# Kernel tuning notes

Measured on AMD Instinct MI355X. Metric: run time of the kernel, lower is better.

The kernel has to match this reference:

```python
import jax, jax.numpy as jnp
import numpy as np

D_MODEL = 1024
N_HEADS = 16
D_KEYS = 64
GROUP_POSITIONS = [list(range(g * 32, (g + 1) * 32)) for g in range(4)]


def _make_tables(group_positions, dim):
    # InGroup table: pe[j,i] = (j/Lg) * L0 / 10000^(2*(i//2)/dim)
    L0 = len(group_positions[0])
    rows = []
    for grp in group_positions:
        Lg = len(grp)
        for j in range(Lg):
            rows.append([j / Lg * L0 / np.power(10000.0, 2 * (i // 2) / dim) for i in range(dim)])
    pe = np.array(rows)
    ingroup = np.concatenate([np.sin(pe[:, 0::2]), np.cos(pe[:, 1::2])], axis=1).astype(np.float32)
    # Sequence (group) table: pe[j,i] = grp[0] / 10000^(j/Lg), constant over i
    rows = []
    for grp in group_positions:
        Lg = len(grp)
        for j in range(Lg):
            rows.append([grp[0] / np.power(10000.0, j / Lg) for _ in range(dim)])
    pe = np.array(rows)
    seq = np.concatenate([np.sin(pe[:, 0::2]), np.cos(pe[:, 1::2])], axis=1).astype(np.float32)
    return jnp.asarray(ingroup), jnp.asarray(seq)


def setup_inputs() -> dict:
    key = jax.random.key(0)
    ks = jax.random.split(key, 12)
    B, L, S = 64, 128, 128
    dqk = D_KEYS * N_HEADS
    sc_in = 1.0 / np.sqrt(D_MODEL)
    sc_out = 1.0 / np.sqrt(dqk)
    inp = {
        "queries": jax.random.normal(ks[0], (B, L, D_MODEL), jnp.float32),
        "keys": jax.random.normal(ks[1], (B, S, D_MODEL), jnp.float32),
        "values": jax.random.normal(ks[2], (B, S, D_MODEL), jnp.float32),
        "attn_mask": jnp.zeros((B, 1, L, S), dtype=bool),
        "Wq": jax.random.normal(ks[3], (D_MODEL, dqk), jnp.float32) * sc_in,
        "bq": jnp.zeros((dqk,), jnp.float32),
        "Wk": jax.random.normal(ks[4], (D_MODEL, dqk), jnp.float32) * sc_in,
        "bk": jnp.zeros((dqk,), jnp.float32),
        "Wv": jax.random.normal(ks[5], (D_MODEL, dqk), jnp.float32) * sc_in,
        "bv": jnp.zeros((dqk,), jnp.float32),
        "Wo": jax.random.normal(ks[6], (dqk, D_MODEL), jnp.float32) * sc_out,
        "bo": jnp.zeros((D_MODEL,), jnp.float32),
    }
    pos_ingroup, pos_seq = _make_tables(GROUP_POSITIONS, D_KEYS)
    inp["pos_ingroup"] = pos_ingroup  # [n_pos, d_keys]
    inp["pos_seq"] = pos_seq          # [n_pos, d_keys]
    return inp


def _rope(x, pos):
    # x: [B, H, L, D]; pos: [L, D]
    sin, cos = jnp.split(pos, 2, axis=-1)
    sin_pos = jnp.stack([sin, sin], axis=-1).reshape(pos.shape)
    cos_pos = jnp.stack([cos, cos], axis=-1).reshape(pos.shape)
    rot = jnp.stack([-x[..., 1::2], x[..., ::2]], axis=-1).reshape(x.shape)
    return x * cos_pos + rot * sin_pos


def reference(queries, keys, values, attn_mask, Wq, bq, Wk, bk, Wv, bv, Wo, bo, pos_ingroup, pos_seq):
    B, L, _ = queries.shape
    S = keys.shape[1]
    H, E = N_HEADS, D_KEYS
    q = (queries @ Wq + bq).reshape(B, L, H, E).transpose(0, 2, 1, 3)  # [B,H,L,E]
    k = (keys @ Wk + bk).reshape(B, S, H, E).transpose(0, 2, 1, 3)
    v = (values @ Wv + bv).reshape(B, S, H, E).transpose(0, 2, 1, 3)
    # group-sequence in-group RoPE, then group RoPE (tables gathered at arange positions)
    q = _rope(_rope(q, pos_ingroup[:L]), pos_seq[:L])
    k = _rope(_rope(k, pos_ingroup[:S]), pos_seq[:S])
    # inner full attention on [B,L,H,E] layout
    scale = 1.0 / jnp.sqrt(jnp.asarray(E, q.dtype))
    scores = jnp.einsum("bhle,bhse->bhls", q, k) * scale
    scores = jnp.where(attn_mask, jnp.asarray(-jnp.inf, scores.dtype), scores)
    attn = jax.nn.softmax(scores, axis=-1)  # [B,H,L,S]
    out = jnp.einsum("bhls,bhsd->blhd", attn, v).reshape(B, L, H * E)
    return out @ Wo + bo, attn
```

## Files before the change

kernel.cpp:

```cpp
#include <hip/hip_runtime.h>
#include <cstdint>

typedef float f32x4 __attribute__((ext_vector_type(4)));
typedef __bf16 bf16x8 __attribute__((ext_vector_type(8)));
typedef unsigned short u16x8 __attribute__((ext_vector_type(8)));

typedef __attribute__((address_space(3))) uint32_t lds_u32;
typedef __attribute__((address_space(1))) const uint32_t glb_u32;

#define GLOAD_LDS16(gp, lp) \
  __builtin_amdgcn_global_load_lds((glb_u32*)(uintptr_t)(gp), (lds_u32*)(uintptr_t)(lp), 16, 0, 0)

__device__ inline unsigned short f2bf(float f) {
  union { float f; uint32_t u; } v; v.f = f;
  uint32_t u = v.u;
  return (unsigned short)((u + 0x7fffu + ((u >> 16) & 1u)) >> 16);
}

__global__ void prep_w(const float* __restrict__ wq, const float* __restrict__ wk,
                       const float* __restrict__ wv, const float* __restrict__ wo,
                       unsigned short* __restrict__ wt)
{
  __shared__ float t[64][65];
  const int z = blockIdx.z;
  const float* W = (z == 0) ? wq : (z == 1) ? wk : (z == 2) ? wv : wo;
  unsigned short* Wt = wt + (size_t)z * 1048576;
  const int n0 = blockIdx.x * 64, k0 = blockIdx.y * 64;
  const int tx = threadIdx.x & 63, ty = threadIdx.x >> 6;
#pragma unroll
  for (int i = 0; i < 16; i++) {
    int row = i * 4 + ty;
    t[row][tx] = W[(size_t)(k0 + row) * 1024 + n0 + tx];
  }
  __syncthreads();
#pragma unroll
  for (int i = 0; i < 16; i++) {
    int row = i * 4 + ty;
    Wt[(size_t)(n0 + row) * 1024 + k0 + tx] = f2bf(t[tx][row]);
  }
}

__global__ void comb_kernel(const float* __restrict__ ing, const float* __restrict__ seq,
                            float* __restrict__ cosc, float* __restrict__ sinc)
{
  int idx = blockIdx.x * 256 + threadIdx.x;
  int j = idx >> 5, i = idx & 31;
  float s1 = ing[j * 64 + i], c1 = ing[j * 64 + 32 + i];
  float s2 = seq[j * 64 + i], c2 = seq[j * 64 + 32 + i];
  cosc[idx] = c1 * c2 - s1 * s2;
  sinc[idx] = s1 * c2 + c1 * s2;
}

__global__ void cvt_kernel(const float* __restrict__ q, const float* __restrict__ k,
                           const float* __restrict__ v, unsigned short* __restrict__ dst)
{
  const int z = blockIdx.z;
  const float* src = (z == 0) ? q : (z == 1) ? k : v;
  unsigned short* d = dst + (size_t)z * 8388608;
  size_t i = ((size_t)blockIdx.x * 256 + threadIdx.x) * 4;
  float4 f = *(const float4*)&src[i];
  ushort4 o;
  o.x = f2bf(f.x); o.y = f2bf(f.y); o.z = f2bf(f.z); o.w = f2bf(f.w);
  *(ushort4*)&d[i] = o;
}

__global__ __launch_bounds__(256, 2)
void gemm_bt(const unsigned short* __restrict__ Abase,
             const unsigned short* __restrict__ Bbase,
             const float* __restrict__ b0, const float* __restrict__ b1,
             const float* __restrict__ b2,
             unsigned short* __restrict__ qb, unsigned short* __restrict__ kb,
             unsigned short* __restrict__ vtb,
             float* __restrict__ outf,
             const float* __restrict__ cosc, const float* __restrict__ sinc,
             int final_mode)
{
  __shared__ __attribute__((aligned(16))) unsigned short Sh[2][8192];
  unsigned short* As = &Sh[0][0];
  unsigned short* Bs = &Sh[1][0];

  const int tid = threadIdx.x;
  const int lane = tid & 63;
  const int wave = tid >> 6;
  const int quad = lane >> 4;
  const int l15 = lane & 15;

  const int z = blockIdx.z;
  const int tileM = blockIdx.x * 128;
  const int tileN = blockIdx.y * 128;
  const int K = 1024;

  const unsigned short* A = Abase + (size_t)z * (8192u * 1024u);
  const unsigned short* B = Bbase + (size_t)z * (1024u * 1024u);

  const int wm = (wave >> 1) * 64;
  const int wn = (wave & 1) * 64;

  f32x4 acc[4][4];
#pragma unroll
  for (int a = 0; a < 4; a++)
#pragma unroll
    for (int n = 0; n < 4; n++)
      acc[a][n] = (f32x4){0.f, 0.f, 0.f, 0.f};

  for (int k0 = 0; k0 < K; k0 += 64) {
#pragma unroll
    for (int cc = 0; cc < 4; cc++) {
      int c = wave * 4 + cc;
      int s = c * 64 + lane;
      int row = s >> 3;
      int gc = (s & 7) ^ (row & 7);
      const unsigned short* ga = A + (size_t)(tileM + row) * K + k0 + gc * 8;
      const unsigned short* gb = B + (size_t)(tileN + row) * K + k0 + gc * 8;
      GLOAD_LDS16(ga, &As[c * 512]);
      GLOAD_LDS16(gb, &Bs[c * 512]);
    }
    __syncthreads();

#pragma unroll
    for (int ks = 0; ks < 2; ks++) {
      bf16x8 af[4], bfr[4];
#pragma unroll
      for (int a = 0; a < 4; a++) {
        int r = wm + a * 16 + l15;
        int cp = (ks * 4 + quad) ^ (r & 7);
        af[a] = *(const bf16x8*)&As[(r * 8 + cp) * 8];
      }
#pragma unroll
      for (int n = 0; n < 4; n++) {
        int r = wn + n * 16 + l15;
        int cp = (ks * 4 + quad) ^ (r & 7);
        bfr[n] = *(const bf16x8*)&Bs[(r * 8 + cp) * 8];
      }
#pragma unroll
      for (int a = 0; a < 4; a++)
#pragma unroll
        for (int n = 0; n < 4; n++)
          acc[a][n] = __builtin_amdgcn_mfma_f32_16x16x32_bf16(af[a], bfr[n], acc[a][n], 0, 0, 0);
    }
    __syncthreads();
  }

  if (final_mode) {
#pragma unroll
    for (int n = 0; n < 4; n++) {
      int cg = tileN + wn + n * 16 + l15;
      float bias = b0[cg];
#pragma unroll
      for (int a = 0; a < 4; a++)
#pragma unroll
        for (int reg = 0; reg < 4; reg++) {
          int r = tileM + wm + a * 16 + quad * 4 + reg;
          outf[(size_t)r * 1024 + cg] = acc[a][n][reg] + bias;
        }
    }
  } else {
    const float* bias = (z == 0) ? b0 : (z == 1) ? b1 : b2;
    unsigned short* outq = (z == 0) ? qb : kb;
    unsigned short* flat = &Sh[0][0];

#pragma unroll
    for (int n = 0; n < 4; n++) {
      int lcg = wn + n * 16 + l15;
      float bv_ = bias[tileN + lcg];
      int e = lcg & 63;
#pragma unroll
      for (int a = 0; a < 4; a++)
#pragma unroll
        for (int reg = 0; reg < 4; reg++) {
          int l = wm + a * 16 + quad * 4 + reg;
          float v = acc[a][n][reg] + bv_;
          unsigned short ov;
          int f;
          if (z == 2) {
            ov = f2bf(v);
            f = lcg * 128 + l;
            f ^= ((f >> 7) & 15) << 3;
          } else {
            float other = __shfl_xor(v, 1);
            float cs = cosc[l * 32 + (e >> 1)];
            float sn = sinc[l * 32 + (e >> 1)];
            ov = f2bf(v * cs + ((e & 1) ? other : -other) * sn);
            f = ((lcg >> 6) << 13) + (l << 6) + e;
            f ^= ((f >> 8) & 7) << 3;
          }
          flat[f] = ov;
        }
    }
    __syncthreads();

    unsigned short* gout = ((z == 2) ? vtb : outq) +
                           ((size_t)(tileM >> 7) * 16 + (tileN >> 6)) * 8192;
#pragma unroll
    for (int c = 0; c < 8; c++) {
      int f0 = tid * 64 + c * 8;
      int s0 = (z == 2) ? (f0 ^ (((f0 >> 7) & 15) << 3))
                        : (f0 ^ (((f0 >> 8) & 7) << 3));
      *(u16x8*)&gout[f0] = *(const u16x8*)&flat[s0];
    }
  }
}

__global__ __launch_bounds__(256, 2)
void attn_kernel(const unsigned short* __restrict__ qb,
                 const unsigned short* __restrict__ kb,
                 const unsigned short* __restrict__ vtb,
                 const unsigned char* __restrict__ mask,
                 float* __restrict__ attn_out,
                 unsigned short* __restrict__ ob)
{
  __shared__ __attribute__((aligned(16))) unsigned short Pb[128 * 136];
  const int tid = threadIdx.x;
  const int lane = tid & 63;
  const int wave = tid >> 6;
  const int quad = lane >> 4;
  const int l15 = lane & 15;
  const int bh = blockIdx.x;
  const int b = bh >> 4;
  const int h = bh & 15;

  const unsigned short* q = qb + (size_t)bh * 128 * 64;
  const unsigned short* k = kb + (size_t)bh * 128 * 64;
  const unsigned short* vt = vtb + (size_t)bh * 64 * 128;

  f32x4 sacc[2][8];
#pragma unroll
  for (int mt = 0; mt < 2; mt++)
#pragma unroll
    for (int nt = 0; nt < 8; nt++)
      sacc[mt][nt] = (f32x4){0.f, 0.f, 0.f, 0.f};

#pragma unroll
  for (int ks = 0; ks < 2; ks++) {
    bf16x8 aq[2], bk[8];
#pragma unroll
    for (int mt = 0; mt < 2; mt++)
      aq[mt] = *(const bf16x8*)&q[(size_t)(wave * 32 + mt * 16 + l15) * 64 + ks * 32 + quad * 8];
#pragma unroll
    for (int nt = 0; nt < 8; nt++)
      bk[nt] = *(const bf16x8*)&k[(size_t)(nt * 16 + l15) * 64 + ks * 32 + quad * 8];
#pragma unroll
    for (int mt = 0; mt < 2; mt++)
#pragma unroll
      for (int nt = 0; nt < 8; nt++)
        sacc[mt][nt] = __builtin_amdgcn_mfma_f32_16x16x32_bf16(aq[mt], bk[nt], sacc[mt][nt], 0, 0, 0);
  }

  const float scale = 0.125f;
#pragma unroll
  for (int mt = 0; mt < 2; mt++) {
#pragma unroll
    for (int reg = 0; reg < 4; reg++) {
      int r = wave * 32 + mt * 16 + quad * 4 + reg;
      const unsigned char* mrow = mask + ((size_t)b * 128 + r) * 128;
      float sv[8];
#pragma unroll
      for (int nt = 0; nt < 8; nt++) {
        float x = sacc[mt][nt][reg] * scale;
        if (mrow[nt * 16 + l15]) x = -__builtin_inff();
        sv[nt] = x;
      }
      float m = sv[0];
#pragma unroll
      for (int nt = 1; nt < 8; nt++) m = fmaxf(m, sv[nt]);
#pragma unroll
      for (int off = 1; off < 16; off <<= 1) m = fmaxf(m, __shfl_xor(m, off));
      float s = 0.f;
#pragma unroll
      for (int nt = 0; nt < 8; nt++) { sv[nt] = __expf(sv[nt] - m); s += sv[nt]; }
#pragma unroll
      for (int off = 1; off < 16; off <<= 1) s += __shfl_xor(s, off);
      float inv = 1.0f / s;
      float* arow = attn_out + ((size_t)bh * 128 + r) * 128;
#pragma unroll
      for (int nt = 0; nt < 8; nt++) {
        float p = sv[nt] * inv;
        arow[nt * 16 + l15] = p;
        Pb[r * 136 + nt * 16 + l15] = f2bf(p);
      }
    }
  }
  __syncthreads();

  f32x4 oacc[2][4];
#pragma unroll
  for (int mt = 0; mt < 2; mt++)
#pragma unroll
    for (int nt = 0; nt < 4; nt++)
      oacc[mt][nt] = (f32x4){0.f, 0.f, 0.f, 0.f};

#pragma unroll
  for (int ks = 0; ks < 4; ks++) {
    bf16x8 bv[4], ap[2];
#pragma unroll
    for (int nt = 0; nt < 4; nt++)
      bv[nt] = *(const bf16x8*)&vt[(size_t)(nt * 16 + l15) * 128 + ks * 32 + quad * 8];
#pragma unroll
    for (int mt = 0; mt < 2; mt++)
      ap[mt] = *(const bf16x8*)&Pb[(size_t)(wave * 32 + mt * 16 + l15) * 136 + ks * 32 + quad * 8];
#pragma unroll
    for (int mt = 0; mt < 2; mt++)
#pragma unroll
      for (int nt = 0; nt < 4; nt++)
        oacc[mt][nt] = __builtin_amdgcn_mfma_f32_16x16x32_bf16(ap[mt], bv[nt], oacc[mt][nt], 0, 0, 0);
  }

#pragma unroll
  for (int mt = 0; mt < 2; mt++)
#pragma unroll
    for (int nt = 0; nt < 4; nt++)
#pragma unroll
      for (int reg = 0; reg < 4; reg++) {
        int r = wave * 32 + mt * 16 + quad * 4 + reg;
        int e = nt * 16 + l15;
        ob[((size_t)b * 128 + r) * 1024 + h * 64 + e] = f2bf(oacc[mt][nt][reg]);
      }
}

extern "C" void kernel_launch(void* const* d_in, const int* in_sizes, int n_in,
                              void* d_out, int out_size, void* d_ws, size_t ws_size,
                              hipStream_t stream)
{
  const float* queries = (const float*)d_in[0];
  const float* keys    = (const float*)d_in[1];
  const float* values  = (const float*)d_in[2];
  const unsigned char* mask = (const unsigned char*)d_in[3];
  const float* Wq = (const float*)d_in[4];
  const float* bq = (const float*)d_in[5];
  const float* Wk = (const float*)d_in[6];
  const float* bk = (const float*)d_in[7];
  const float* Wv = (const float*)d_in[8];
  const float* bv = (const float*)d_in[9];
  const float* Wo = (const float*)d_in[10];
  const float* bo = (const float*)d_in[11];
  const float* ping = (const float*)d_in[12];
  const float* pseq = (const float*)d_in[13];

  float* out  = (float*)d_out;
  float* attn = out + 8388608;
  unsigned short* Xbf = (unsigned short*)attn;

  char* ws = (char*)d_ws;
  unsigned short* Wt  = (unsigned short*)(ws);
  float* cosc = (float*)(ws + 8388608);
  float* sinc = (float*)(ws + 8388608 + 16384);
  unsigned short* qbuf = (unsigned short*)(ws + 8421376);
  unsigned short* kbuf = (unsigned short*)(ws + 8421376 + 16777216);
  unsigned short* vtbuf= (unsigned short*)(ws + 8421376 + 2*16777216);
  unsigned short* obuf = (unsigned short*)(ws + 8421376 + 3*16777216);

  prep_w<<<dim3(16, 16, 4), 256, 0, stream>>>(Wq, Wk, Wv, Wo, Wt);
  comb_kernel<<<16, 256, 0, stream>>>(ping, pseq, cosc, sinc);
  cvt_kernel<<<dim3(8192, 1, 3), 256, 0, stream>>>(queries, keys, values, Xbf);
  gemm_bt<<<dim3(64, 8, 3), 256, 0, stream>>>(Xbf, Wt, bq, bk, bv,
                                              qbuf, kbuf, vtbuf, nullptr,
                                              cosc, sinc, 0);
  attn_kernel<<<dim3(1024), 256, 0, stream>>>(qbuf, kbuf, vtbuf, mask, attn, obuf);
  gemm_bt<<<dim3(64, 8, 1), 256, 0, stream>>>(obuf, Wt + 3 * 1048576, bo, bo, bo,
                                              qbuf, kbuf, vtbuf, out,
                                              cosc, sinc, 1);
}
```

Measured before the change: 338.3 us.

## Fuse fp32-to-bf16 input conversion into QKV projection GEMM

Removes the separate conversion kernel that wrote bf16 copies of queries/keys/values, and adds a dedicated QKV GEMM that loads fp32 activations straight into LDS (swizzled) and converts to bf16 when building MFMA fragments. This drops a full read+write pass over the activations and one launch. In exchange the A tile in LDS doubles in size (fp32). Each of the 8 column-tile blocks now re-reads fp32 A, twice the bytes of the bf16 copy, and conversion work is repeated per block.

After: 345.8 us. 1.02x slower.

```diff
diff --git a/kernel.cpp b/kernel.cpp
--- a/kernel.cpp
+++ b/kernel.cpp
@@ -51,17 +51,134 @@
   sinc[idx] = s1 * c2 + c1 * s2;
 }
 
-__global__ void cvt_kernel(const float* __restrict__ q, const float* __restrict__ k,
-                           const float* __restrict__ v, unsigned short* __restrict__ dst)
-{
+__global__ __launch_bounds__(256, 2)
+void gemm_qkv(const float* __restrict__ qf, const float* __restrict__ kf,
+              const float* __restrict__ vf,
+              const unsigned short* __restrict__ Bbase,
+              const float* __restrict__ b0, const float* __restrict__ b1,
+              const float* __restrict__ b2,
+              unsigned short* __restrict__ qb, unsigned short* __restrict__ kb,
+              unsigned short* __restrict__ vtb,
+              const float* __restrict__ cosc, const float* __restrict__ sinc)
+{
+  __shared__ __attribute__((aligned(16))) float Asf[8192];
+  __shared__ __attribute__((aligned(16))) unsigned short Bs[8192];
+
+  const int tid = threadIdx.x;
+  const int lane = tid & 63;
+  const int wave = tid >> 6;
+  const int quad = lane >> 4;
+  const int l15 = lane & 15;
+
   const int z = blockIdx.z;
-  const float* src = (z == 0) ? q : (z == 1) ? k : v;
-  unsigned short* d = dst + (size_t)z * 8388608;
-  size_t i = ((size_t)blockIdx.x * 256 + threadIdx.x) * 4;
-  float4 f = *(const float4*)&src[i];
-  ushort4 o;
-  o.x = f2bf(f.x); o.y = f2bf(f.y); o.z = f2bf(f.z); o.w = f2bf(f.w);
-  *(ushort4*)&d[i] = o;
+  const int tileM = blockIdx.x * 128;
+  const int tileN = blockIdx.y * 128;
+  const int K = 1024;
+
+  const float* A = (z == 0) ? qf : (z == 1) ? kf : vf;
+  const unsigned short* B = Bbase + (size_t)z * (1024u * 1024u);
+
+  const int wm = (wave >> 1) * 64;
+  const int wn = (wave & 1) * 64;
+
+  f32x4 acc[4][4];
+#pragma unroll
+  for (int a = 0; a < 4; a++)
+#pragma unroll
+    for (int n = 0; n < 4; n++)
+      acc[a][n] = (f32x4){0.f, 0.f, 0.f, 0.f};
+
+  for (int k0 = 0; k0 < K; k0 += 64) {
+#pragma unroll
+    for (int cc = 0; cc < 8; cc++) {
+      int c = wave * 8 + cc;
+      int g = c * 64 + lane;
+      int row = g >> 4;
+      int gc = (g & 15) ^ (row & 15);
+      const float* ga = A + (size_t)(tileM + row) * 1024 + k0 + gc * 4;
+      GLOAD_LDS16(ga, &Asf[c * 256]);
+    }
+#pragma unroll
+    for (int cc = 0; cc < 4; cc++) {
+      int c = wave * 4 + cc;
+      int s = c * 64 + lane;
+      int row = s >> 3;
+      int gc = (s & 7) ^ (row & 7);
+      const unsigned short* gb = B + (size_t)(tileN + row) * K + k0 + gc * 8;
+      GLOAD_LDS16(gb, &Bs[c * 512]);
+    }
+    __syncthreads();
+
+#pragma unroll
+    for (int ks = 0; ks < 2; ks++) {
+      bf16x8 af[4], bfr[4];
+#pragma unroll
+      for (int a = 0; a < 4; a++) {
+        int r = wm + a * 16 + l15;
+        int L0 = ks * 8 + quad * 2;
+        f32x4 fa = *(const f32x4*)&Asf[(r * 16 + (L0 ^ l15)) * 4];
+        f32x4 fb = *(const f32x4*)&Asf[(r * 16 + ((L0 + 1) ^ l15)) * 4];
+        af[a] = (bf16x8){(__bf16)fa[0], (__bf16)fa[1], (__bf16)fa[2], (__bf16)fa[3],
+                         (__bf16)fb[0], (__bf16)fb[1], (__bf16)fb[2], (__bf16)fb[3]};
+      }
+#pragma unroll
+      for (int n = 0; n < 4; n++) {
+        int r = wn + n * 16 + l15;
+        int cp = (ks * 4 + quad) ^ (r & 7);
+        bfr[n] = *(const bf16x8*)&Bs[(r * 8 + cp) * 8];
+      }
+#pragma unroll
+      for (int a = 0; a < 4; a++)
+#pragma unroll
+        for (int n = 0; n < 4; n++)
+          acc[a][n] = __builtin_amdgcn_mfma_f32_16x16x32_bf16(af[a], bfr[n], acc[a][n], 0, 0, 0);
+    }
+    __syncthreads();
+  }
+
+  const float* bias = (z == 0) ? b0 : (z == 1) ? b1 : b2;
+  unsigned short* outq = (z == 0) ? qb : kb;
+  unsigned short* flat = (unsigned short*)Asf;
+
+#pragma unroll
+  for (int n = 0; n < 4; n++) {
+    int lcg = wn + n * 16 + l15;
+    float bv_ = bias[tileN + lcg];
+    int e = lcg & 63;
+#pragma unroll
+    for (int a = 0; a < 4; a++)
+#pragma unroll
+      for (int reg = 0; reg < 4; reg++) {
+        int l = wm + a * 16 + quad * 4 + reg;
+        float v = acc[a][n][reg] + bv_;
+        unsigned short ov;
+        int f;
+        if (z == 2) {
+          ov = f2bf(v);
+          f = lcg * 128 + l;
+          f ^= ((f >> 7) & 15) << 3;
+        } else {
+          float other = __shfl_xor(v, 1);
+          float cs = cosc[l * 32 + (e >> 1)];
+          float sn = sinc[l * 32 + (e >> 1)];
+          ov = f2bf(v * cs + ((e & 1) ? other : -other) * sn);
+          f = ((lcg >> 6) << 13) + (l << 6) + e;
+          f ^= ((f >> 8) & 7) << 4;
+        }
+        flat[f] = ov;
+      }
+  }
+  __syncthreads();
+
+  unsigned short* gout = ((z == 2) ? vtb : outq) +
+                         ((size_t)(tileM >> 7) * 16 + (tileN >> 6)) * 8192;
+#pragma unroll
+  for (int c = 0; c < 8; c++) {
+    int f0 = tid * 64 + c * 8;
+    int s0 = (z == 2) ? (f0 ^ (((f0 >> 7) & 15) << 3))
+                      : (f0 ^ (((f0 >> 8) & 7) << 4));
+    *(u16x8*)&gout[f0] = *(const u16x8*)&flat[s0];
+  }
 }
 
 __global__ __launch_bounds__(256, 2)
@@ -338,7 +455,6 @@
 
   float* out  = (float*)d_out;
   float* attn = out + 8388608;
-  unsigned short* Xbf = (unsigned short*)attn;
 
   char* ws = (char*)d_ws;
   unsigned short* Wt  = (unsigned short*)(ws);
@@ -351,10 +467,9 @@
 
   prep_w<<<dim3(16, 16, 4), 256, 0, stream>>>(Wq, Wk, Wv, Wo, Wt);
   comb_kernel<<<16, 256, 0, stream>>>(ping, pseq, cosc, sinc);
-  cvt_kernel<<<dim3(8192, 1, 3), 256, 0, stream>>>(queries, keys, values, Xbf);
-  gemm_bt<<<dim3(64, 8, 3), 256, 0, stream>>>(Xbf, Wt, bq, bk, bv,
-                                              qbuf, kbuf, vtbuf, nullptr,
-                                              cosc, sinc, 0);
+  gemm_qkv<<<dim3(64, 8, 3), 256, 0, stream>>>(queries, keys, values, Wt,
+                                               bq, bk, bv,
+                                               qbuf, kbuf, vtbuf, cosc, sinc);
   attn_kernel<<<dim3(1024), 256, 0, stream>>>(qbuf, kbuf, vtbuf, mask, attn, obuf);
   gemm_bt<<<dim3(64, 8, 1), 256, 0, stream>>>(obuf, Wt + 3 * 1048576, bo, bo, bo,
                                               qbuf, kbuf, vtbuf, out,
```

## Merge prep kernels into one launch, stage output GEMM stores via LDS

Applied to the files above, without the earlier changes.

The three preprocessing kernels (input bf16 conversion, weight transpose/convert, RoPE table combine) are merged into a single launch that dispatches on block index, removing two kernel launches and their gaps. The final GEMM epilogue now writes its fp32 tile into LDS in two halves and stores coalesced 16-byte vectors to global memory instead of scattered 4-byte stores. The XOR swizzle for q/k staging is also widened to shift LDS bank conflicts. The cost is extra barriers in the epilogue and branchy block dispatch in the merged kernel.

Measured after the change: 338.8 us. No clear change (+0.1%).

```diff
diff --git a/kernel.cpp b/kernel.cpp
--- a/kernel.cpp
+++ b/kernel.cpp
@@ -17,51 +17,55 @@
   return (unsigned short)((u + 0x7fffu + ((u >> 16) & 1u)) >> 16);
 }
 
-__global__ void prep_w(const float* __restrict__ wq, const float* __restrict__ wk,
-                       const float* __restrict__ wv, const float* __restrict__ wo,
-                       unsigned short* __restrict__ wt)
+__global__ void prep_all(const float* __restrict__ q, const float* __restrict__ k,
+                         const float* __restrict__ v,
+                         const float* __restrict__ wq, const float* __restrict__ wk,
+                         const float* __restrict__ wv, const float* __restrict__ wo,
+                         const float* __restrict__ ing, const float* __restrict__ seq,
+                         unsigned short* __restrict__ dst, unsigned short* __restrict__ wt,
+                         float* __restrict__ cosc, float* __restrict__ sinc)
 {
   __shared__ float t[64][65];
-  const int z = blockIdx.z;
-  const float* W = (z == 0) ? wq : (z == 1) ? wk : (z == 2) ? wv : wo;
-  unsigned short* Wt = wt + (size_t)z * 1048576;
-  const int n0 = blockIdx.x * 64, k0 = blockIdx.y * 64;
-  const int tx = threadIdx.x & 63, ty = threadIdx.x >> 6;
-#pragma unroll
-  for (int i = 0; i < 16; i++) {
-    int row = i * 4 + ty;
-    t[row][tx] = W[(size_t)(k0 + row) * 1024 + n0 + tx];
-  }
-  __syncthreads();
-#pragma unroll
-  for (int i = 0; i < 16; i++) {
-    int row = i * 4 + ty;
-    Wt[(size_t)(n0 + row) * 1024 + k0 + tx] = f2bf(t[tx][row]);
-  }
-}
-
-__global__ void comb_kernel(const float* __restrict__ ing, const float* __restrict__ seq,
-                            float* __restrict__ cosc, float* __restrict__ sinc)
-{
-  int idx = blockIdx.x * 256 + threadIdx.x;
-  int j = idx >> 5, i = idx & 31;
-  float s1 = ing[j * 64 + i], c1 = ing[j * 64 + 32 + i];
-  float s2 = seq[j * 64 + i], c2 = seq[j * 64 + 32 + i];
-  cosc[idx] = c1 * c2 - s1 * s2;
-  sinc[idx] = s1 * c2 + c1 * s2;
-}
-
-__global__ void cvt_kernel(const float* __restrict__ q, const float* __restrict__ k,
-                           const float* __restrict__ v, unsigned short* __restrict__ dst)
-{
-  const int z = blockIdx.z;
-  const float* src = (z == 0) ? q : (z == 1) ? k : v;
-  unsigned short* d = dst + (size_t)z * 8388608;
-  size_t i = ((size_t)blockIdx.x * 256 + threadIdx.x) * 4;
-  float4 f = *(const float4*)&src[i];
-  ushort4 o;
-  o.x = f2bf(f.x); o.y = f2bf(f.y); o.z = f2bf(f.z); o.w = f2bf(f.w);
-  *(ushort4*)&d[i] = o;
+  const int bx = blockIdx.x;
+  const int tid = threadIdx.x;
+
+  if (bx < 24576) {
+    int z = bx >> 13;
+    int b8 = bx & 8191;
+    const float* src = (z == 0) ? q : (z == 1) ? k : v;
+    unsigned short* d = dst + (size_t)z * 8388608;
+    size_t i = ((size_t)b8 * 256 + tid) * 4;
+    float4 f = *(const float4*)&src[i];
+    ushort4 o;
+    o.x = f2bf(f.x); o.y = f2bf(f.y); o.z = f2bf(f.z); o.w = f2bf(f.w);
+    *(ushort4*)&d[i] = o;
+  } else if (bx < 25600) {
+    int pb = bx - 24576;
+    int z = pb >> 8;
+    int rem = pb & 255;
+    const float* W = (z == 0) ? wq : (z == 1) ? wk : (z == 2) ? wv : wo;
+    unsigned short* Wt = wt + (size_t)z * 1048576;
+    const int n0 = (rem & 15) * 64, k0 = (rem >> 4) * 64;
+    const int tx = tid & 63, ty = tid >> 6;
+#pragma unroll
+    for (int i = 0; i < 16; i++) {
+      int row = i * 4 + ty;
+      t[row][tx] = W[(size_t)(k0 + row) * 1024 + n0 + tx];
+    }
+    __syncthreads();
+#pragma unroll
+    for (int i = 0; i < 16; i++) {
+      int row = i * 4 + ty;
+      Wt[(size_t)(n0 + row) * 1024 + k0 + tx] = f2bf(t[tx][row]);
+    }
+  } else {
+    int idx = (bx - 25600) * 256 + tid;
+    int j = idx >> 5, i = idx & 31;
+    float s1 = ing[j * 64 + i], c1 = ing[j * 64 + 32 + i];
+    float s2 = seq[j * 64 + i], c2 = seq[j * 64 + 32 + i];
+    cosc[idx] = c1 * c2 - s1 * s2;
+    sinc[idx] = s1 * c2 + c1 * s2;
+  }
 }
 
 __global__ __launch_bounds__(256, 2)
@@ -142,17 +146,32 @@
   }
 
   if (final_mode) {
-#pragma unroll
-    for (int n = 0; n < 4; n++) {
-      int cg = tileN + wn + n * 16 + l15;
-      float bias = b0[cg];
-#pragma unroll
-      for (int a = 0; a < 4; a++)
-#pragma unroll
-        for (int reg = 0; reg < 4; reg++) {
-          int r = tileM + wm + a * 16 + quad * 4 + reg;
-          outf[(size_t)r * 1024 + cg] = acc[a][n][reg] + bias;
+    float* flatf = (float*)&Sh[0][0];
+#pragma unroll
+    for (int h = 0; h < 2; h++) {
+      __syncthreads();
+      if ((wave >> 1) == h) {
+#pragma unroll
+        for (int n = 0; n < 4; n++) {
+          int lcg = wn + n * 16 + l15;
+          float bias = b0[tileN + lcg];
+#pragma unroll
+          for (int a = 0; a < 4; a++)
+#pragma unroll
+            for (int reg = 0; reg < 4; reg++) {
+              int lrow = a * 16 + quad * 4 + reg;
+              flatf[lrow * 128 + lcg] = acc[a][n][reg] + bias;
+            }
         }
+      }
+      __syncthreads();
+#pragma unroll
+      for (int c = 0; c < 8; c++) {
+        int ff = (c * 256 + tid) * 4;
+        int row = ff >> 7, col = ff & 127;
+        *(f32x4*)&outf[(size_t)(tileM + h * 64 + row) * 1024 + tileN + col] =
+            *(const f32x4*)&flatf[ff];
+      }
     }
   } else {
     const float* bias = (z == 0) ? b0 : (z == 1) ? b1 : b2;
@@ -182,7 +201,7 @@
             float sn = sinc[l * 32 + (e >> 1)];
             ov = f2bf(v * cs + ((e & 1) ? other : -other) * sn);
             f = ((lcg >> 6) << 13) + (l << 6) + e;
-            f ^= ((f >> 8) & 7) << 3;
+            f ^= ((f >> 8) & 7) << 4;
           }
           flat[f] = ov;
         }
@@ -195,7 +214,7 @@
     for (int c = 0; c < 8; c++) {
       int f0 = tid * 64 + c * 8;
       int s0 = (z == 2) ? (f0 ^ (((f0 >> 7) & 15) << 3))
-                        : (f0 ^ (((f0 >> 8) & 7) << 3));
+                        : (f0 ^ (((f0 >> 8) & 7) << 4));
       *(u16x8*)&gout[f0] = *(const u16x8*)&flat[s0];
     }
   }
@@ -349,9 +368,9 @@
   unsigned short* vtbuf= (unsigned short*)(ws + 8421376 + 2*16777216);
   unsigned short* obuf = (unsigned short*)(ws + 8421376 + 3*16777216);
 
-  prep_w<<<dim3(16, 16, 4), 256, 0, stream>>>(Wq, Wk, Wv, Wo, Wt);
-  comb_kernel<<<16, 256, 0, stream>>>(ping, pseq, cosc, sinc);
-  cvt_kernel<<<dim3(8192, 1, 3), 256, 0, stream>>>(queries, keys, values, Xbf);
+  prep_all<<<dim3(25616), 256, 0, stream>>>(queries, keys, values,
+                                            Wq, Wk, Wv, Wo, ping, pseq,
+                                            Xbf, Wt, cosc, sinc);
   gemm_bt<<<dim3(64, 8, 3), 256, 0, stream>>>(Xbf, Wt, bq, bk, bv,
                                               qbuf, kbuf, vtbuf, nullptr,
                                               cosc, sinc, 0);
```
